# Kernel tuning notes

Measured on AMD Instinct MI355X. Metric: run time of the kernel, lower is better.

Reference implementation:

```python
import jax, jax.numpy as jnp
import numpy as np


def _tsallis15_probs(x):
    """entmax-1.5 / Tsallis alpha=1.5 mapping over axis=1. x: [n, d] logits."""
    x = (x - jnp.max(x, axis=1, keepdims=True)) * 0.5
    xs = -jnp.sort(-x, axis=1)                       # descending sort  [n, d]
    d = x.shape[1]
    rho = jnp.arange(1, d + 1, dtype=x.dtype)        # 1..d
    mean = jnp.cumsum(xs, axis=1) / rho
    mean_sq = jnp.cumsum(xs * xs, axis=1) / rho
    ss = rho * (mean_sq - mean * mean)
    delta = (1.0 - ss) / rho
    tau = mean - jnp.sqrt(jnp.clip(delta, 0.0))
    support_size = jnp.sum(tau <= xs, axis=1)        # [n]
    tau_star = jnp.take_along_axis(tau, (support_size - 1)[:, None], axis=1)
    y = jnp.clip(x - tau_star, 0.0)
    return y * y                                     # p*, rows sum to 1


def setup_inputs() -> dict:
    key = jax.random.key(0)
    k1, k2 = jax.random.split(key)
    inp = jax.random.normal(k1, (2048, 32000), dtype=jnp.float32)
    target = jax.random.randint(k2, (2048,), 0, 32000, dtype=jnp.int64)
    return {"input": inp, "target": target}


def reference(input, target):
    n = input.shape[0]
    p_star = _tsallis15_probs(input)
    # omega_tsallis15: (1 - sum p^{3/2}) / 0.75 per row
    loss = (1.0 - jnp.sum(p_star * jnp.sqrt(p_star), axis=1)) / 0.75
    # scatter_add(-1) at the target class, then <p* - e_y, x> per row
    pm = p_star.at[jnp.arange(n), target].add(-1.0)
    loss = loss + jnp.einsum('ij,ij->i', pm, input)
    # reduction='elementwise_mean', ignore_index=-100 (<0: no masking)
    return jnp.sum(loss) / n
```

## Files before the change

kernel.cpp:

```cpp
#include <hip/hip_runtime.h>
#include <math.h>

#define BLOCK 512
#define NWAVES (BLOCK / 64)
#define CAND_CAP 6144
#define NREG 12

__device__ __forceinline__ float waveReduceMax(float v) {
#pragma unroll
    for (int off = 32; off > 0; off >>= 1)
        v = fmaxf(v, __shfl_down(v, off, 64));
    return v;
}
__device__ __forceinline__ float waveReduceSum(float v) {
#pragma unroll
    for (int off = 32; off > 0; off >>= 1)
        v += __shfl_down(v, off, 64);
    return v;
}

__global__ __launch_bounds__(BLOCK, 8) void tsallis15_kernel(
    const float* __restrict__ x, const int* __restrict__ tgt,
    float* __restrict__ out, int n, int d, float inv_n)
{
    __shared__ float s_cand[CAND_CAP];
    __shared__ float s_red[NWAVES];
    __shared__ int   s_cnt;
    __shared__ float s_bcast;

    const int row  = blockIdx.x;
    const int t    = threadIdx.x;
    const int lane = t & 63;
    const int wave = t >> 6;
    const float* __restrict__ xr = x + (size_t)row * (size_t)d;
    const float4* __restrict__ xr4 = reinterpret_cast<const float4*>(xr);
    const int d4 = d >> 2;

    if (t == 0) s_cnt = 0;

    float m = -INFINITY;
    for (int i = t; i < d4; i += BLOCK) {
        float4 v = xr4[i];
        m = fmaxf(m, fmaxf(fmaxf(v.x, v.y), fmaxf(v.z, v.w)));
    }
    {
        int e = (d4 << 2) + t;
        if (e < d) m = fmaxf(m, xr[e]);
    }
    m = waveReduceMax(m);
    if (lane == 0) s_red[wave] = m;
    __syncthreads();
    if (wave == 0) {
        float v = (lane < NWAVES) ? s_red[lane] : -INFINITY;
        v = waveReduceMax(v);
        if (lane == 0) s_bcast = v;
    }
    __syncthreads();
    const float rowmax = s_bcast;
    const float thr = rowmax - 2.0f;

    for (int i = t; i < d4; i += BLOCK) {
        float4 v = xr4[i];
        float mx4 = fmaxf(fmaxf(v.x, v.y), fmaxf(v.z, v.w));
        unsigned long long any = __ballot(mx4 >= thr);
        if (any) {
            float vals[4] = { v.x, v.y, v.z, v.w };
#pragma unroll
            for (int c = 0; c < 4; ++c) {
                float vv = vals[c];
                bool pred = (vv >= thr);
                unsigned long long mask = __ballot(pred);
                if (mask) {
                    int base;
                    if (lane == 0) base = atomicAdd(&s_cnt, __popcll(mask));
                    base = __shfl(base, 0, 64);
                    if (pred) {
                        int pos = base + (int)__popcll(mask & ((1ull << lane) - 1ull));
                        if (pos < CAND_CAP) s_cand[pos] = (vv - rowmax) * 0.5f;
                    }
                }
            }
        }
    }
    {
        int e = (d4 << 2) + t;
        float vv = (e < d) ? xr[e] : -INFINITY;
        bool pred = (vv >= thr);
        unsigned long long mask = __ballot(pred);
        if (mask) {
            int base;
            if (lane == 0) base = atomicAdd(&s_cnt, __popcll(mask));
            base = __shfl(base, 0, 64);
            if (pred) {
                int pos = base + (int)__popcll(mask & ((1ull << lane) - 1ull));
                if (pos < CAND_CAP) s_cand[pos] = (vv - rowmax) * 0.5f;
            }
        }
    }
    __syncthreads();

    if (wave == 0) {
        const int k = min(s_cnt, CAND_CAP);

        float xt = 0.0f;
        if (lane == 0) xt = xr[tgt[row]];

        float ur[NREG];
#pragma unroll
        for (int j = 0; j < NREG; ++j) {
            int idx = lane + 64 * j;
            ur[j] = (idx < k) ? s_cand[idx] : -1e30f;
        }

        float lo = -1.0f, hi = 0.0f;
        for (int it = 0; it < 18; ++it) {
            float tau = 0.5f * (lo + hi);
            float acc = 0.0f;
#pragma unroll
            for (int j = 0; j < NREG; ++j) {
                float u = ur[j] - tau;
                acc += (u > 0.0f) ? u * u : 0.0f;
            }
            for (int j = 64 * NREG + lane; j < k; j += 64) {
                float u = s_cand[j] - tau;
                if (u > 0.0f) acc += u * u;
            }
            float tot = waveReduceSum(acc);
            tot = __shfl(tot, 0, 64);
            if (tot >= 1.0f) lo = tau; else hi = tau;
        }
        const float tau_b = 0.5f * (lo + hi);

        float s1 = 0.0f, s2 = 0.0f, sc = 0.0f;
#pragma unroll
        for (int j = 0; j < NREG; ++j) {
            float u = ur[j];
            if (u > tau_b) { s1 += u; s2 += u * u; sc += 1.0f; }
        }
        for (int j = 64 * NREG + lane; j < k; j += 64) {
            float u = s_cand[j];
            if (u > tau_b) { s1 += u; s2 += u * u; sc += 1.0f; }
        }
        s1 = waveReduceSum(s1); s1 = __shfl(s1, 0, 64);
        s2 = waveReduceSum(s2); s2 = __shfl(s2, 0, 64);
        sc = waveReduceSum(sc); sc = __shfl(sc, 0, 64);
        float mean  = s1 / sc;
        float ss    = s2 - s1 * mean;
        float delta = (1.0f - ss) / sc;
        if (delta < 0.0f) delta = 0.0f;
        const float tau_star = mean - sqrtf(delta);

        float p32 = 0.0f, dot = 0.0f;
#pragma unroll
        for (int j = 0; j < NREG; ++j) {
            float u = ur[j] - tau_star;
            if (u > 0.0f) {
                float p = u * u;
                p32 += p * u;
                dot += p * (2.0f * ur[j] + rowmax);
            }
        }
        for (int j = 64 * NREG + lane; j < k; j += 64) {
            float uc = s_cand[j];
            float u  = uc - tau_star;
            if (u > 0.0f) {
                float p = u * u;
                p32 += p * u;
                dot += p * (2.0f * uc + rowmax);
            }
        }
        p32 = waveReduceSum(p32);
        dot = waveReduceSum(dot);
        if (lane == 0) {
            float loss = (1.0f - p32) * (4.0f / 3.0f) + dot - xt;
            atomicAdd(out, loss * inv_n);
        }
    }
}

extern "C" void kernel_launch(void* const* d_in, const int* in_sizes, int n_in,
                              void* d_out, int out_size, void* d_ws, size_t ws_size,
                              hipStream_t stream) {
    const float* x   = (const float*)d_in[0];
    const int*   tgt = (const int*)d_in[1];
    float*       out = (float*)d_out;

    const int n = in_sizes[1];
    const int d = in_sizes[0] / n;

    hipMemsetAsync(out, 0, (size_t)out_size * sizeof(float), stream);
    tsallis15_kernel<<<n, BLOCK, 0, stream>>>(x, tgt, out, n, d, 1.0f / (float)n);
}
```

Measured before the change: 403.0 us.

## Cache row in registers with 1024-thread blocks to avoid second global pass

Raises the block size to 1024 and has each thread load its slice of the row (8 float4 per thread) into registers once, then reuses those registers for both the max reduction and candidate filtering instead of re-reading the row from global memory. The target logit load is also hoisted to the start. This removes the second read of each row but depends on d fitting within BLOCK*NV*4 = 32768 elements, and it raises register pressure while dropping the per-float4 early-skip ballot.

```diff
diff --git a/kernel.cpp b/kernel.cpp
--- a/kernel.cpp
+++ b/kernel.cpp
@@ -1,8 +1,9 @@
 #include <hip/hip_runtime.h>
 #include <math.h>
 
-#define BLOCK 512
+#define BLOCK 1024
 #define NWAVES (BLOCK / 64)
+#define NV 8
 #define CAND_CAP 6144
 #define NREG 12
 
@@ -33,20 +34,31 @@
     const int lane = t & 63;
     const int wave = t >> 6;
     const float* __restrict__ xr = x + (size_t)row * (size_t)d;
-    const float4* __restrict__ xr4 = reinterpret_cast<const float4*>(xr);
-    const int d4 = d >> 2;
 
     if (t == 0) s_cnt = 0;
 
+    float xt = 0.0f;
+    if (t == 0) xt = xr[tgt[row]];
+
+    float4 r[NV];
+#pragma unroll
+    for (int i = 0; i < NV; ++i) {
+        int e = (i * BLOCK + t) * 4;
+        if (e + 4 <= d) {
+            r[i] = *reinterpret_cast<const float4*>(xr + e);
+        } else {
+            float4 v = make_float4(-INFINITY, -INFINITY, -INFINITY, -INFINITY);
+            if (e < d)     v.x = xr[e];
+            if (e + 1 < d) v.y = xr[e + 1];
+            if (e + 2 < d) v.z = xr[e + 2];
+            r[i] = v;
+        }
+    }
+
     float m = -INFINITY;
-    for (int i = t; i < d4; i += BLOCK) {
-        float4 v = xr4[i];
-        m = fmaxf(m, fmaxf(fmaxf(v.x, v.y), fmaxf(v.z, v.w)));
-    }
-    {
-        int e = (d4 << 2) + t;
-        if (e < d) m = fmaxf(m, xr[e]);
-    }
+#pragma unroll
+    for (int i = 0; i < NV; ++i)
+        m = fmaxf(m, fmaxf(fmaxf(r[i].x, r[i].y), fmaxf(r[i].z, r[i].w)));
     m = waveReduceMax(m);
     if (lane == 0) s_red[wave] = m;
     __syncthreads();
@@ -57,43 +69,24 @@
     }
     __syncthreads();
     const float rowmax = s_bcast;
+
     const float thr = rowmax - 2.0f;
-
-    for (int i = t; i < d4; i += BLOCK) {
-        float4 v = xr4[i];
-        float mx4 = fmaxf(fmaxf(v.x, v.y), fmaxf(v.z, v.w));
-        unsigned long long any = __ballot(mx4 >= thr);
-        if (any) {
-            float vals[4] = { v.x, v.y, v.z, v.w };
 #pragma unroll
-            for (int c = 0; c < 4; ++c) {
-                float vv = vals[c];
-                bool pred = (vv >= thr);
-                unsigned long long mask = __ballot(pred);
-                if (mask) {
-                    int base;
-                    if (lane == 0) base = atomicAdd(&s_cnt, __popcll(mask));
-                    base = __shfl(base, 0, 64);
-                    if (pred) {
-                        int pos = base + (int)__popcll(mask & ((1ull << lane) - 1ull));
-                        if (pos < CAND_CAP) s_cand[pos] = (vv - rowmax) * 0.5f;
-                    }
+    for (int i = 0; i < NV; ++i) {
+        float vals[4] = { r[i].x, r[i].y, r[i].z, r[i].w };
+#pragma unroll
+        for (int c = 0; c < 4; ++c) {
+            float v = vals[c];
+            bool pred = (v >= thr);
+            unsigned long long mask = __ballot(pred);
+            if (mask) {
+                int base;
+                if (lane == 0) base = atomicAdd(&s_cnt, __popcll(mask));
+                base = __shfl(base, 0, 64);
+                if (pred) {
+                    int pos = base + (int)__popcll(mask & ((1ull << lane) - 1ull));
+                    if (pos < CAND_CAP) s_cand[pos] = (v - rowmax) * 0.5f;
                 }
-            }
-        }
-    }
-    {
-        int e = (d4 << 2) + t;
-        float vv = (e < d) ? xr[e] : -INFINITY;
-        bool pred = (vv >= thr);
-        unsigned long long mask = __ballot(pred);
-        if (mask) {
-            int base;
-            if (lane == 0) base = atomicAdd(&s_cnt, __popcll(mask));
-            base = __shfl(base, 0, 64);
-            if (pred) {
-                int pos = base + (int)__popcll(mask & ((1ull << lane) - 1ull));
-                if (pos < CAND_CAP) s_cand[pos] = (vv - rowmax) * 0.5f;
             }
         }
     }
@@ -101,9 +94,6 @@
 
     if (wave == 0) {
         const int k = min(s_cnt, CAND_CAP);
-
-        float xt = 0.0f;
-        if (lane == 0) xt = xr[tgt[row]];
 
         float ur[NREG];
 #pragma unroll
```

New measurement: 372.3 us. 1.08x faster.
